# Optimization experiments

Measured on AMD Instinct MI355X. Metric: run time of the kernel, lower is better.

Reference implementation:

```python
import jax, jax.numpy as jnp
import numpy as np

N, E, D, H, L = 50000, 800000, 64, 128, 3  # nodes, edges, embed dim, mlp hidden (2*D), layers
HDIM, EDIM, G = 8, 8, 10
EPS_MSG = 1e-7
BN_EPS = 1e-5
LN_EPS = 1e-5


def setup_inputs() -> dict:
    key = jax.random.key(0)
    ks = jax.random.split(key, 12)
    s = lambda f: 1.0 / np.sqrt(f)
    return {
        "x": jax.random.normal(ks[0], (N, HDIM), jnp.float32),
        "edge_index": jax.random.randint(ks[1], (2, E), 0, N, dtype=jnp.int32),
        "edge_attr": jax.random.normal(ks[2], (E, EDIM), jnp.float32),
        "node_W": jax.random.normal(ks[3], (HDIM, D), jnp.float32) * s(HDIM),
        "node_b": jnp.zeros((D,), jnp.float32),
        "edge_W": jax.random.normal(ks[4], (EDIM, D), jnp.float32) * s(EDIM),
        "edge_b": jnp.zeros((D,), jnp.float32),
        "bn_gamma": jnp.ones((L, D), jnp.float32),
        "bn_beta": jnp.zeros((L, D), jnp.float32),
        "t": jnp.ones((L,), jnp.float32),
        "W1": jax.random.normal(ks[5], (L, D, H), jnp.float32) * s(D),
        "b1": jnp.zeros((L, H), jnp.float32),
        "ln_g": jnp.ones((L, H), jnp.float32),
        "ln_b": jnp.zeros((L, H), jnp.float32),
        "W2": jax.random.normal(ks[6], (L, H, D), jnp.float32) * s(H),
        "b2": jnp.zeros((L, D), jnp.float32),
        "num_graphs": G,
    }


def _layer(h, src, dst, e, g, b, t_i, W1i, b1i, lg, lb, W2i, b2i):
    # DeepGCNLayer 'res+': out = x + conv(relu(BN(x)))
    mu = h.mean(0)
    var = h.var(0)  # biased, as torch BN normalization
    hn = jax.nn.relu((h - mu) / jnp.sqrt(var + BN_EPS) * g + b)
    # GENConv message: relu(x_j + edge_attr) + eps
    msg = jax.nn.relu(hn[src] + e) + EPS_MSG  # [E, D]
    # softmax aggregation per destination node, per channel, with temperature t
    logits = msg * t_i
    m = jax.ops.segment_max(logits, dst, num_segments=N)
    m = jnp.where(jnp.isfinite(m), m, 0.0)
    a = jnp.exp(logits - m[dst])
    denom = jax.ops.segment_sum(a, dst, num_segments=N)
    agg = jax.ops.segment_sum(a * msg, dst, num_segments=N)
    agg = agg / jnp.maximum(denom, 1e-16)
    out = agg + hn  # GENConv root residual
    # GENConv MLP [D, 2D, D]: Linear -> LayerNorm -> ReLU -> Linear
    y = out @ W1i + b1i
    mu2 = y.mean(-1, keepdims=True)
    var2 = y.var(-1, keepdims=True)
    y = (y - mu2) / jnp.sqrt(var2 + LN_EPS) * lg + lb
    y = jax.nn.relu(y)
    y = y @ W2i + b2i
    return h + y


def reference(x, edge_index, edge_attr, node_W, node_b, edge_W, edge_b,
              bn_gamma, bn_beta, t, W1, b1, ln_g, ln_b, W2, b2, num_graphs):
    h = x @ node_W + node_b
    e = edge_attr @ edge_W + edge_b
    src, dst = edge_index[0], edge_index[1]
    for i in range(L):
        h = _layer(h, src, dst, e, bn_gamma[i], bn_beta[i], t[i],
                   W1[i], b1[i], ln_g[i], ln_b[i], W2[i], b2[i])
    return h.reshape(num_graphs, -1, D)
```

## Files before the change

### kernel.cpp

```cpp
#include <hip/hip_runtime.h>
#include <hip/hip_bf16.h>
#include <hip/hip_fp16.h>

constexpr int HDIM = 8;
constexpr int EDIM = 8;

typedef _Float16 half8 __attribute__((ext_vector_type(8)));
typedef _Float16 h2f16 __attribute__((ext_vector_type(2)));
typedef float f32x4 __attribute__((ext_vector_type(4)));
union H8U { uint4 u; half8 h; };
union H2U { unsigned u; h2f16 h; };

__device__ __forceinline__ unsigned pack2h(float a, float b) {
  __half2 h = __floats2half2_rn(a, b);
  union { __half2 h2; unsigned u; } u;
  u.h2 = h;
  return u.u;
}

__device__ __forceinline__ h2f16 u2h(unsigned v) {
  H2U u; u.u = v; return u.h;
}

__global__ __launch_bounds__(256) void init_h_stats_kernel(
    const float* __restrict__ x, const float* __restrict__ W, const float* __restrict__ b,
    unsigned short* __restrict__ h, float* __restrict__ sums, int* __restrict__ deg, int n) {
  __shared__ float reds[256], redq[256];
  int tid = threadIdx.x, lane = tid & 63;
  int gtid = blockIdx.x * 256 + tid;
  for (int i = gtid; i < n; i += 512 * 256) deg[i] = 0;
  float wc[HDIM];
#pragma unroll
  for (int k = 0; k < HDIM; ++k) wc[k] = W[k * 64 + lane];
  float bc = b[lane];
  float s = 0.f, q = 0.f;
  int total = n * 64;
  for (int gid = gtid; gid < total; gid += 512 * 256) {
    int row = gid >> 6;
    const float* xr = x + (size_t)row * HDIM;
    float acc = bc;
#pragma unroll
    for (int k = 0; k < HDIM; ++k) acc = fmaf(xr[k], wc[k], acc);
    h[gid] = __half_as_ushort(__float2half(acc));
    s += acc;
    q = fmaf(acc, acc, q);
  }
  reds[tid] = s; redq[tid] = q;
  __syncthreads();
  if (tid < 64) {
    float S = reds[tid] + reds[64 + tid] + reds[128 + tid] + reds[192 + tid];
    float Q = redq[tid] + redq[64 + tid] + redq[128 + tid] + redq[192 + tid];
    int slot = blockIdx.x & 7;
    atomicAdd(&sums[slot * 128 + tid], S);
    atomicAdd(&sums[slot * 128 + 64 + tid], Q);
  }
}

__global__ void deg_kernel(const int* __restrict__ dst, int* __restrict__ deg,
                           int* __restrict__ idxw, int E) {
  int e = blockIdx.x * 256 + threadIdx.x;
  if (e < E) idxw[e] = atomicAdd(&deg[dst[e]], 1);
}

__global__ __launch_bounds__(256) void scan_part_kernel(const int* __restrict__ deg,
                                                        int* __restrict__ partials, int n) {
  __shared__ int sh[256];
  int tid = threadIdx.x, idx = blockIdx.x * 256 + tid;
  int v = (idx < n) ? deg[idx] : 0;
  sh[tid] = v;
  __syncthreads();
  for (int o = 128; o > 0; o >>= 1) {
    if (tid < o) sh[tid] += sh[tid + o];
    __syncthreads();
  }
  if (tid == 0) partials[blockIdx.x] = sh[0];
}

__global__ __launch_bounds__(1024) void scan_top_kernel(int* __restrict__ partials, int nb) {
  __shared__ int sh[1024];
  int tid = threadIdx.x;
  int v = (tid < nb) ? partials[tid] : 0;
  sh[tid] = v;
  __syncthreads();
  for (int o = 1; o < 1024; o <<= 1) {
    int a = (tid >= o) ? sh[tid - o] : 0;
    __syncthreads();
    sh[tid] += a;
    __syncthreads();
  }
  if (tid < nb) partials[tid] = sh[tid] - v;
}

__global__ __launch_bounds__(256) void scan_fill_kernel(
    const int* __restrict__ deg, const int* __restrict__ partials,
    int* __restrict__ rowstart, int n, int total) {
  __shared__ int sh[256];
  int tid = threadIdx.x, idx = blockIdx.x * 256 + tid;
  int v = (idx < n) ? deg[idx] : 0;
  sh[tid] = v;
  __syncthreads();
  for (int o = 1; o < 256; o <<= 1) {
    int a = (tid >= o) ? sh[tid - o] : 0;
    __syncthreads();
    sh[tid] += a;
    __syncthreads();
  }
  if (idx < n) rowstart[idx] = partials[blockIdx.x] + sh[tid] - v;
  if (blockIdx.x == 0 && tid == 0) rowstart[n] = total;
}

__global__ void fill_kernel(const int* __restrict__ src, const int* __restrict__ dst,
                            const int* __restrict__ idxw, const int* __restrict__ rowstart,
                            const float* __restrict__ edge_attr, char* __restrict__ recs, int E) {
  int e = blockIdx.x * 256 + threadIdx.x;
  if (e >= E) return;
  int d = dst[e];
  int slot = rowstart[d] + idxw[e];
  const float4* ap = (const float4*)(edge_attr + (size_t)e * EDIM);
  float4 a = ap[0], c = ap[1];
  uint4 rv;
  rv.x = pack2h(a.x, a.y);
  rv.y = pack2h(a.z, a.w);
  rv.z = pack2h(c.x, c.y);
  rv.w = pack2h(c.z, c.w);
  char* rb = recs + (size_t)slot * 32;
  *(uint4*)rb = rv;
  *(int*)(rb + 16) = src[e];
}

__global__ __launch_bounds__(256) void aggregate_kernel(
    const unsigned short* __restrict__ h, const float* __restrict__ sums,
    const float* __restrict__ bn_g, const float* __restrict__ bn_b,
    const int* __restrict__ rowstart, const char* __restrict__ recs,
    const float* __restrict__ edge_W, const float* __restrict__ edge_b,
    const float* __restrict__ t, unsigned short* __restrict__ out, int n, float invN) {
  int lane = threadIdx.x & 63;
  int node = blockIdx.x * 4 + (threadIdx.x >> 6);
  if (node >= n) return;
  float ssum = 0.f, qsum = 0.f;
#pragma unroll
  for (int k = 0; k < 8; ++k) {
    ssum += sums[k * 128 + lane];
    qsum += sums[k * 128 + 64 + lane];
  }
  float mu = ssum * invN;
  float var = qsum * invN - mu * mu;
  float aa = rsqrtf(var + 1e-5f) * bn_g[lane];
  float cc = bn_b[lane] - mu * aa;
  h2f16 wc2[4];
#pragma unroll
  for (int k = 0; k < 4; ++k) {
    H2U u;
    u.u = pack2h(edge_W[(2 * k) * 64 + lane], edge_W[(2 * k + 1) * 64 + lane]);
    wc2[k] = u.h;
  }
  float eb = edge_b[lane];
  float tt2 = t[0] * 1.44269504088896f;
  int s0 = __builtin_amdgcn_readfirstlane(rowstart[node]);
  int s1 = __builtin_amdgcn_readfirstlane(rowstart[node + 1]);
  const char* hB = (const char*)h;
  const unsigned lane2 = (unsigned)lane * 2u;
  float hd;
  {
    unsigned o = (unsigned)node * 128u + lane2;
    hd = fmaxf(fmaf(__half2float(__ushort_as_half(*(const unsigned short*)(hB + o))), aa, cc), 0.f);
  }
  float den0 = 0.f, num0 = 0.f, den1 = 0.f, num1 = 0.f;
#define EDGE_STEP(HU, RV, DEN, NUM)                                            \
  {                                                                            \
    float ev = __builtin_amdgcn_fdot2(u2h(RV.x), wc2[0], eb, false);           \
    ev = __builtin_amdgcn_fdot2(u2h(RV.y), wc2[1], ev, false);                 \
    ev = __builtin_amdgcn_fdot2(u2h(RV.z), wc2[2], ev, false);                 \
    ev = __builtin_amdgcn_fdot2(u2h(RV.w), wc2[3], ev, false);                 \
    float hnv = fmaxf(fmaf(__half2float(__ushort_as_half(HU)), aa, cc), 0.f);  \
    float m = fmaxf(hnv + ev, 0.f);                                            \
    float p = exp2f(m * tt2);                                                  \
    DEN += p;                                                                  \
    NUM = fmaf(p, m, NUM);                                                     \
  }
#define GATHER(I) (*(const unsigned short*)(hB + ((unsigned)(I) * 128u + lane2)))
  int j = s0;
  for (; j + 8 <= s1; j += 8) {
    unsigned jb = (unsigned)j * 32u;
    uint4 r0 = *(const uint4*)(recs + jb);
    uint4 r1 = *(const uint4*)(recs + jb + 32);
    uint4 r2 = *(const uint4*)(recs + jb + 64);
    uint4 r3 = *(const uint4*)(recs + jb + 96);
    uint4 r4 = *(const uint4*)(recs + jb + 128);
    uint4 r5 = *(const uint4*)(recs + jb + 160);
    uint4 r6 = *(const uint4*)(recs + jb + 192);
    uint4 r7 = *(const uint4*)(recs + jb + 224);
    int i0 = *(const int*)(recs + jb + 16);
    int i1 = *(const int*)(recs + jb + 48);
    int i2 = *(const int*)(recs + jb + 80);
    int i3 = *(const int*)(recs + jb + 112);
    int i4 = *(const int*)(recs + jb + 144);
    int i5 = *(const int*)(recs + jb + 176);
    int i6 = *(const int*)(recs + jb + 208);
    int i7 = *(const int*)(recs + jb + 240);
    unsigned short u0 = GATHER(i0);
    unsigned short u1 = GATHER(i1);
    unsigned short u2 = GATHER(i2);
    unsigned short u3 = GATHER(i3);
    unsigned short u4 = GATHER(i4);
    unsigned short u5 = GATHER(i5);
    unsigned short u6 = GATHER(i6);
    unsigned short u7 = GATHER(i7);
    EDGE_STEP(u0, r0, den0, num0)
    EDGE_STEP(u1, r1, den1, num1)
    EDGE_STEP(u2, r2, den0, num0)
    EDGE_STEP(u3, r3, den1, num1)
    EDGE_STEP(u4, r4, den0, num0)
    EDGE_STEP(u5, r5, den1, num1)
    EDGE_STEP(u6, r6, den0, num0)
    EDGE_STEP(u7, r7, den1, num1)
  }
  for (; j + 4 <= s1; j += 4) {
    unsigned jb = (unsigned)j * 32u;
    uint4 r0 = *(const uint4*)(recs + jb);
    uint4 r1 = *(const uint4*)(recs + jb + 32);
    uint4 r2 = *(const uint4*)(recs + jb + 64);
    uint4 r3 = *(const uint4*)(recs + jb + 96);
    int i0 = *(const int*)(recs + jb + 16);
    int i1 = *(const int*)(recs + jb + 48);
    int i2 = *(const int*)(recs + jb + 80);
    int i3 = *(const int*)(recs + jb + 112);
    unsigned short u0 = GATHER(i0);
    unsigned short u1 = GATHER(i1);
    unsigned short u2 = GATHER(i2);
    unsigned short u3 = GATHER(i3);
    EDGE_STEP(u0, r0, den0, num0)
    EDGE_STEP(u1, r1, den1, num1)
    EDGE_STEP(u2, r2, den0, num0)
    EDGE_STEP(u3, r3, den1, num1)
  }
  for (; j < s1; ++j) {
    unsigned jb = (unsigned)j * 32u;
    uint4 r0 = *(const uint4*)(recs + jb);
    int i0 = *(const int*)(recs + jb + 16);
    unsigned short u0 = GATHER(i0);
    EDGE_STEP(u0, r0, den0, num0)
  }
#undef GATHER
#undef EDGE_STEP
  float den = den0 + den1, num = num0 + num1;
  float res = num / fmaxf(den, 1e-16f) + 1e-7f + hd;
  {
    unsigned o = (unsigned)node * 128u + lane2;
    *(unsigned short*)((char*)out + o) = __half_as_ushort(__float2half(res));
  }
}

__global__ __launch_bounds__(256) void mlp_mfma_kernel(
    const unsigned short* __restrict__ outv, const unsigned short* __restrict__ h_in,
    const float* __restrict__ W1, const float* __restrict__ b1,
    const float* __restrict__ lng, const float* __restrict__ lnb,
    const float* __restrict__ W2, const float* __restrict__ b2,
    unsigned short* __restrict__ hout16, float* __restrict__ hout32,
    float* __restrict__ nextsums, int n) {
  __shared__ uint4 lds[2560];
  const int tid = threadIdx.x;
  const int wv = tid >> 6, l = tid & 63;
  const int n0 = blockIdx.x * 64;
  uint4* XA = lds;
  uint4* WB = lds + 512;
  uint4* ZF = lds + 1536;
#pragma unroll
  for (int i = 0; i < 2; ++i) {
    int c = tid + i * 256;
    int node = c >> 3, k8 = c & 7;
    int nd = n0 + node;
    uint4 u;
    if (nd < n) {
      u = *(const uint4*)(outv + (size_t)nd * 64 + k8 * 8);
    } else {
      u = make_uint4(0, 0, 0, 0);
    }
    int mt = node >> 4, kt = k8 >> 2;
    int lanep = ((k8 & 3) << 4) | (node & 15);
    XA[(mt * 2 + kt) * 64 + lanep] = u;
  }
#pragma unroll
  for (int i = 0; i < 4; ++i) {
    int c = tid + i * 256;
    int fid = c >> 6, lp = c & 63;
    int nt = fid >> 1, kt = fid & 1;
    int ncol = (nt << 4) | (lp & 15);
    int k0 = kt * 32 + (lp >> 4) * 8;
    half8 hv;
#pragma unroll
    for (int j = 0; j < 8; ++j) hv[j] = (_Float16)W1[(size_t)(k0 + j) * 128 + ncol];
    H8U u; u.h = hv;
    WB[fid * 64 + lp] = u.u;
  }
  __syncthreads();
  f32x4 cfr[8];
#pragma unroll
  for (int nt = 0; nt < 8; ++nt) cfr[nt] = (f32x4){0.f, 0.f, 0.f, 0.f};
  {
    H8U a0, a1;
    a0.u = XA[(wv * 2 + 0) * 64 + l];
    a1.u = XA[(wv * 2 + 1) * 64 + l];
#pragma unroll
    for (int nt = 0; nt < 8; ++nt) {
      H8U b0, b1u;
      b0.u = WB[(nt * 2 + 0) * 64 + l];
      b1u.u = WB[(nt * 2 + 1) * 64 + l];
      cfr[nt] = __builtin_amdgcn_mfma_f32_16x16x32_f16(a0.h, b0.h, cfr[nt], 0, 0, 0);
      cfr[nt] = __builtin_amdgcn_mfma_f32_16x16x32_f16(a1.h, b1u.h, cfr[nt], 0, 0, 0);
    }
  }
  int col = l & 15;
  float s4[4] = {0.f, 0.f, 0.f, 0.f}, q4[4] = {0.f, 0.f, 0.f, 0.f};
#pragma unroll
  for (int nt = 0; nt < 8; ++nt) {
    float bb = b1[nt * 16 + col];
#pragma unroll
    for (int r = 0; r < 4; ++r) {
      float v = cfr[nt][r] + bb;
      cfr[nt][r] = v;
      s4[r] += v;
      q4[r] = fmaf(v, v, q4[r]);
    }
  }
#pragma unroll
  for (int off = 1; off < 16; off <<= 1) {
#pragma unroll
    for (int r = 0; r < 4; ++r) {
      s4[r] += __shfl_xor(s4[r], off, 64);
      q4[r] += __shfl_xor(q4[r], off, 64);
    }
  }
  float mu4[4], rs4[4];
#pragma unroll
  for (int r = 0; r < 4; ++r) {
    float mu = s4[r] * (1.f / 128.f);
    float var = q4[r] * (1.f / 128.f) - mu * mu;
    mu4[r] = mu;
    rs4[r] = rsqrtf(var + 1e-5f);
  }
  {
    unsigned short* ZB = (unsigned short*)ZF;
#pragma unroll
    for (int nt = 0; nt < 8; ++nt) {
      int ch = nt * 16 + col;
      int kt2 = ch >> 5, kl = ch & 31;
      float g = lng[ch], bb = lnb[ch];
#pragma unroll
      for (int r = 0; r < 4; ++r) {
        int row = (l >> 4) * 4 + r;
        float zv = fmaxf((cfr[nt][r] - mu4[r]) * rs4[r] * g + bb, 0.f);
        int lanep = ((kl >> 3) << 4) | row;
        ZB[((wv * 4 + kt2) * 64 + lanep) * 8 + (kl & 7)] = __half_as_ushort(__float2half(zv));
      }
    }
  }
  __syncthreads();
#pragma unroll
  for (int i = 0; i < 4; ++i) {
    int c = tid + i * 256;
    int fid = c >> 6, lp = c & 63;
    int nt2 = fid >> 2, kt2 = fid & 3;
    int ncol = (nt2 << 4) | (lp & 15);
    int k0 = kt2 * 32 + (lp >> 4) * 8;
    half8 hv;
#pragma unroll
    for (int j = 0; j < 8; ++j) hv[j] = (_Float16)W2[(size_t)(k0 + j) * 64 + ncol];
    H8U u; u.h = hv;
    WB[fid * 64 + lp] = u.u;
  }
  __syncthreads();
  f32x4 dfr[4];
#pragma unroll
  for (int nt2 = 0; nt2 < 4; ++nt2) dfr[nt2] = (f32x4){0.f, 0.f, 0.f, 0.f};
  {
    H8U za[4];
#pragma unroll
    for (int kt2 = 0; kt2 < 4; ++kt2) za[kt2].u = ZF[(wv * 4 + kt2) * 64 + l];
#pragma unroll
    for (int nt2 = 0; nt2 < 4; ++nt2) {
#pragma unroll
      for (int kt2 = 0; kt2 < 4; ++kt2) {
        H8U bu;
        bu.u = WB[(nt2 * 4 + kt2) * 64 + l];
        dfr[nt2] = __builtin_amdgcn_mfma_f32_16x16x32_f16(za[kt2].h, bu.h, dfr[nt2], 0, 0, 0);
      }
    }
  }
  float ssum[4] = {0.f, 0.f, 0.f, 0.f}, qsum[4] = {0.f, 0.f, 0.f, 0.f};
#pragma unroll
  for (int nt2 = 0; nt2 < 4; ++nt2) {
    int ch2 = nt2 * 16 + col;
    float bb = b2[ch2];
#pragma unroll
    for (int r = 0; r < 4; ++r) {
      int nd = n0 + wv * 16 + (l >> 4) * 4 + r;
      if (nd < n) {
        float hv = __half2float(__ushort_as_half(h_in[(size_t)nd * 64 + ch2]));
        float v = hv + dfr[nt2][r] + bb;
        if (hout32 != nullptr) {
          hout32[(size_t)nd * 64 + ch2] = v;
        } else {
          hout16[(size_t)nd * 64 + ch2] = __half_as_ushort(__float2half(v));
        }
        ssum[nt2] += v;
        qsum[nt2] = fmaf(v, v, qsum[nt2]);
      }
    }
  }
  if (nextsums != nullptr) {
#pragma unroll
    for (int nt2 = 0; nt2 < 4; ++nt2) {
      ssum[nt2] += __shfl_xor(ssum[nt2], 16, 64);
      ssum[nt2] += __shfl_xor(ssum[nt2], 32, 64);
      qsum[nt2] += __shfl_xor(qsum[nt2], 16, 64);
      qsum[nt2] += __shfl_xor(qsum[nt2], 32, 64);
    }
    float* SS = (float*)(ZF + wv * 256);
    if (l < 16) {
#pragma unroll
      for (int nt2 = 0; nt2 < 4; ++nt2) {
        SS[nt2 * 16 + l] = ssum[nt2];
        SS[64 + nt2 * 16 + l] = qsum[nt2];
      }
    }
    __syncthreads();
    if (tid < 64) {
      float S = 0.f, Q = 0.f;
#pragma unroll
      for (int w = 0; w < 4; ++w) {
        const float* P = (const float*)(ZF + w * 256);
        S += P[tid];
        Q += P[64 + tid];
      }
      int slot = blockIdx.x & 7;
      atomicAdd(&nextsums[slot * 128 + tid], S);
      atomicAdd(&nextsums[slot * 128 + 64 + tid], Q);
    }
  }
}

extern "C" void kernel_launch(void* const* d_in, const int* in_sizes, int n_in,
                              void* d_out, int out_size, void* d_ws, size_t ws_size,
                              hipStream_t stream) {
  const float* x = (const float*)d_in[0];
  const int* edge_index = (const int*)d_in[1];
  const float* edge_attr = (const float*)d_in[2];
  const float* node_W = (const float*)d_in[3];
  const float* node_b = (const float*)d_in[4];
  const float* edge_W = (const float*)d_in[5];
  const float* edge_b = (const float*)d_in[6];
  const float* bn_g = (const float*)d_in[7];
  const float* bn_b = (const float*)d_in[8];
  const float* t = (const float*)d_in[9];
  const float* W1 = (const float*)d_in[10];
  const float* b1 = (const float*)d_in[11];
  const float* ln_g = (const float*)d_in[12];
  const float* ln_b = (const float*)d_in[13];
  const float* W2 = (const float*)d_in[14];
  const float* b2 = (const float*)d_in[15];

  int N = in_sizes[0] / HDIM;
  int E = in_sizes[1] / 2;
  const int* srcp = edge_index;
  const int* dstp = edge_index + E;

  char* ws = (char*)d_ws;
  size_t off = 0;
  auto alloc = [&](size_t bytes) {
    char* p = ws + off;
    off = (off + bytes + 255) & ~(size_t)255;
    return p;
  };
  int* deg = (int*)alloc((size_t)N * 4);
  int* rowstart = (int*)alloc(((size_t)N + 1) * 4);
  int* idxw = (int*)alloc((size_t)E * 4);
  int* partials = (int*)alloc(1024 * 4);
  float* bnsums = (float*)alloc(3 * 1024 * 4);
  char* recs = (char*)alloc((size_t)E * 32);
  unsigned short* h = (unsigned short*)alloc((size_t)N * 64 * 2);
  unsigned short* outv = (unsigned short*)alloc((size_t)N * 64 * 2);
  (void)ws_size; (void)n_in; (void)out_size;

  int nb = (N + 255) / 256;
  hipMemsetAsync(bnsums, 0, 3 * 1024 * 4, stream);
  init_h_stats_kernel<<<512, 256, 0, stream>>>(x, node_W, node_b, h, bnsums, deg, N);
  deg_kernel<<<(E + 255) / 256, 256, 0, stream>>>(dstp, deg, idxw, E);
  scan_part_kernel<<<nb, 256, 0, stream>>>(deg, partials, N);
  scan_top_kernel<<<1, 1024, 0, stream>>>(partials, nb);
  scan_fill_kernel<<<nb, 256, 0, stream>>>(deg, partials, rowstart, N, E);
  fill_kernel<<<(E + 255) / 256, 256, 0, stream>>>(srcp, dstp, idxw, rowstart, edge_attr, recs, E);

  float invN = 1.0f / (float)N;
  int mlp_blocks = (N + 63) / 64;
  for (int l = 0; l < 3; ++l) {
    aggregate_kernel<<<(N + 3) / 4, 256, 0, stream>>>(
        h, bnsums + l * 1024, bn_g + l * 64, bn_b + l * 64, rowstart, recs,
        edge_W, edge_b, t + l, outv, N, invN);
    unsigned short* h16 = (l == 2) ? nullptr : h;
    float* h32 = (l == 2) ? (float*)d_out : nullptr;
    float* nxt = (l == 2) ? nullptr : (bnsums + (l + 1) * 1024);
    mlp_mfma_kernel<<<mlp_blocks, 256, 0, stream>>>(outv, h, W1 + (size_t)l * 8192, b1 + l * 128,
                                                    ln_g + l * 128, ln_b + l * 128,
                                                    W2 + (size_t)l * 8192, b2 + l * 64,
                                                    h16, h32, nxt, N);
  }
}
```

Baseline: 252.3 us.

## Fuse preprocessing kernels, use nontemporal record loads, two nodes per wave in aggregation

Degree counting moves into the init kernel and deg zeroing into the single memset, made possible by placing bnsums next to deg. The top-level scan is folded into scan_fill, with each block rescanning the partials itself. Together these remove two launches. The aggregate kernel now handles two nodes per wavefront, amortising the BN/weight setup, and loads edge records with nontemporal hints to avoid polluting cache. The risks are lower parallelism in aggregation and the scan_fill assumption that nb is at most 256, which holds for N=50000.

```diff
diff --git a/kernel.cpp b/kernel.cpp
--- a/kernel.cpp
+++ b/kernel.cpp
@@ -8,6 +8,7 @@
 typedef _Float16 half8 __attribute__((ext_vector_type(8)));
 typedef _Float16 h2f16 __attribute__((ext_vector_type(2)));
 typedef float f32x4 __attribute__((ext_vector_type(4)));
+typedef unsigned u32x4 __attribute__((ext_vector_type(4)));
 union H8U { uint4 u; half8 h; };
 union H2U { unsigned u; h2f16 h; };
 
@@ -24,11 +25,13 @@
 
 __global__ __launch_bounds__(256) void init_h_stats_kernel(
     const float* __restrict__ x, const float* __restrict__ W, const float* __restrict__ b,
-    unsigned short* __restrict__ h, float* __restrict__ sums, int* __restrict__ deg, int n) {
+    unsigned short* __restrict__ h, float* __restrict__ sums,
+    const int* __restrict__ dst, int* __restrict__ idxw, int* __restrict__ deg,
+    int n, int E) {
   __shared__ float reds[256], redq[256];
   int tid = threadIdx.x, lane = tid & 63;
   int gtid = blockIdx.x * 256 + tid;
-  for (int i = gtid; i < n; i += 512 * 256) deg[i] = 0;
+  for (int e = gtid; e < E; e += 512 * 256) idxw[e] = atomicAdd(&deg[dst[e]], 1);
   float wc[HDIM];
 #pragma unroll
   for (int k = 0; k < HDIM; ++k) wc[k] = W[k * 64 + lane];
@@ -54,12 +57,6 @@
     atomicAdd(&sums[slot * 128 + tid], S);
     atomicAdd(&sums[slot * 128 + 64 + tid], Q);
   }
-}
-
-__global__ void deg_kernel(const int* __restrict__ dst, int* __restrict__ deg,
-                           int* __restrict__ idxw, int E) {
-  int e = blockIdx.x * 256 + threadIdx.x;
-  if (e < E) idxw[e] = atomicAdd(&deg[dst[e]], 1);
 }
 
 __global__ __launch_bounds__(256) void scan_part_kernel(const int* __restrict__ deg,
@@ -76,36 +73,27 @@
   if (tid == 0) partials[blockIdx.x] = sh[0];
 }
 
-__global__ __launch_bounds__(1024) void scan_top_kernel(int* __restrict__ partials, int nb) {
-  __shared__ int sh[1024];
-  int tid = threadIdx.x;
-  int v = (tid < nb) ? partials[tid] : 0;
-  sh[tid] = v;
-  __syncthreads();
-  for (int o = 1; o < 1024; o <<= 1) {
-    int a = (tid >= o) ? sh[tid - o] : 0;
-    __syncthreads();
-    sh[tid] += a;
-    __syncthreads();
-  }
-  if (tid < nb) partials[tid] = sh[tid] - v;
-}
-
 __global__ __launch_bounds__(256) void scan_fill_kernel(
     const int* __restrict__ deg, const int* __restrict__ partials,
-    int* __restrict__ rowstart, int n, int total) {
+    int* __restrict__ rowstart, int n, int total, int nb) {
+  __shared__ int tp[256];
   __shared__ int sh[256];
   int tid = threadIdx.x, idx = blockIdx.x * 256 + tid;
+  int pv = (tid < nb) ? partials[tid] : 0;
+  tp[tid] = pv;
   int v = (idx < n) ? deg[idx] : 0;
   sh[tid] = v;
   __syncthreads();
   for (int o = 1; o < 256; o <<= 1) {
-    int a = (tid >= o) ? sh[tid - o] : 0;
+    int a1 = (tid >= o) ? tp[tid - o] : 0;
+    int a2 = (tid >= o) ? sh[tid - o] : 0;
     __syncthreads();
-    sh[tid] += a;
+    tp[tid] += a1;
+    sh[tid] += a2;
     __syncthreads();
   }
-  if (idx < n) rowstart[idx] = partials[blockIdx.x] + sh[tid] - v;
+  int base = (blockIdx.x == 0) ? 0 : tp[blockIdx.x - 1];
+  if (idx < n) rowstart[idx] = base + sh[tid] - v;
   if (blockIdx.x == 0 && tid == 0) rowstart[n] = total;
 }
 
@@ -128,38 +116,12 @@
   *(int*)(rb + 16) = src[e];
 }
 
-__global__ __launch_bounds__(256) void aggregate_kernel(
-    const unsigned short* __restrict__ h, const float* __restrict__ sums,
-    const float* __restrict__ bn_g, const float* __restrict__ bn_b,
+__device__ __forceinline__ float agg_one(
+    int node, unsigned lane2, const char* __restrict__ hB,
     const int* __restrict__ rowstart, const char* __restrict__ recs,
-    const float* __restrict__ edge_W, const float* __restrict__ edge_b,
-    const float* __restrict__ t, unsigned short* __restrict__ out, int n, float invN) {
-  int lane = threadIdx.x & 63;
-  int node = blockIdx.x * 4 + (threadIdx.x >> 6);
-  if (node >= n) return;
-  float ssum = 0.f, qsum = 0.f;
-#pragma unroll
-  for (int k = 0; k < 8; ++k) {
-    ssum += sums[k * 128 + lane];
-    qsum += sums[k * 128 + 64 + lane];
-  }
-  float mu = ssum * invN;
-  float var = qsum * invN - mu * mu;
-  float aa = rsqrtf(var + 1e-5f) * bn_g[lane];
-  float cc = bn_b[lane] - mu * aa;
-  h2f16 wc2[4];
-#pragma unroll
-  for (int k = 0; k < 4; ++k) {
-    H2U u;
-    u.u = pack2h(edge_W[(2 * k) * 64 + lane], edge_W[(2 * k + 1) * 64 + lane]);
-    wc2[k] = u.h;
-  }
-  float eb = edge_b[lane];
-  float tt2 = t[0] * 1.44269504088896f;
+    const h2f16* wc2, float eb, float tt2, float aa, float cc) {
   int s0 = __builtin_amdgcn_readfirstlane(rowstart[node]);
   int s1 = __builtin_amdgcn_readfirstlane(rowstart[node + 1]);
-  const char* hB = (const char*)h;
-  const unsigned lane2 = (unsigned)lane * 2u;
   float hd;
   {
     unsigned o = (unsigned)node * 128u + lane2;
@@ -179,25 +141,27 @@
     NUM = fmaf(p, m, NUM);                                                     \
   }
 #define GATHER(I) (*(const unsigned short*)(hB + ((unsigned)(I) * 128u + lane2)))
+#define NT4(OFF) __builtin_nontemporal_load((const u32x4*)(recs + jb + (OFF)))
+#define NTI(OFF) __builtin_nontemporal_load((const int*)(recs + jb + (OFF)))
   int j = s0;
   for (; j + 8 <= s1; j += 8) {
     unsigned jb = (unsigned)j * 32u;
-    uint4 r0 = *(const uint4*)(recs + jb);
-    uint4 r1 = *(const uint4*)(recs + jb + 32);
-    uint4 r2 = *(const uint4*)(recs + jb + 64);
-    uint4 r3 = *(const uint4*)(recs + jb + 96);
-    uint4 r4 = *(const uint4*)(recs + jb + 128);
-    uint4 r5 = *(const uint4*)(recs + jb + 160);
-    uint4 r6 = *(const uint4*)(recs + jb + 192);
-    uint4 r7 = *(const uint4*)(recs + jb + 224);
-    int i0 = *(const int*)(recs + jb + 16);
-    int i1 = *(const int*)(recs + jb + 48);
-    int i2 = *(const int*)(recs + jb + 80);
-    int i3 = *(const int*)(recs + jb + 112);
-    int i4 = *(const int*)(recs + jb + 144);
-    int i5 = *(const int*)(recs + jb + 176);
-    int i6 = *(const int*)(recs + jb + 208);
-    int i7 = *(const int*)(recs + jb + 240);
+    u32x4 r0 = NT4(0);
+    u32x4 r1 = NT4(32);
+    u32x4 r2 = NT4(64);
+    u32x4 r3 = NT4(96);
+    u32x4 r4 = NT4(128);
+    u32x4 r5 = NT4(160);
+    u32x4 r6 = NT4(192);
+    u32x4 r7 = NT4(224);
+    int i0 = NTI(16);
+    int i1 = NTI(48);
+    int i2 = NTI(80);
+    int i3 = NTI(112);
+    int i4 = NTI(144);
+    int i5 = NTI(176);
+    int i6 = NTI(208);
+    int i7 = NTI(240);
     unsigned short u0 = GATHER(i0);
     unsigned short u1 = GATHER(i1);
     unsigned short u2 = GATHER(i2);
@@ -217,14 +181,14 @@
   }
   for (; j + 4 <= s1; j += 4) {
     unsigned jb = (unsigned)j * 32u;
-    uint4 r0 = *(const uint4*)(recs + jb);
-    uint4 r1 = *(const uint4*)(recs + jb + 32);
-    uint4 r2 = *(const uint4*)(recs + jb + 64);
-    uint4 r3 = *(const uint4*)(recs + jb + 96);
-    int i0 = *(const int*)(recs + jb + 16);
-    int i1 = *(const int*)(recs + jb + 48);
-    int i2 = *(const int*)(recs + jb + 80);
-    int i3 = *(const int*)(recs + jb + 112);
+    u32x4 r0 = NT4(0);
+    u32x4 r1 = NT4(32);
+    u32x4 r2 = NT4(64);
+    u32x4 r3 = NT4(96);
+    int i0 = NTI(16);
+    int i1 = NTI(48);
+    int i2 = NTI(80);
+    int i3 = NTI(112);
     unsigned short u0 = GATHER(i0);
     unsigned short u1 = GATHER(i1);
     unsigned short u2 = GATHER(i2);
@@ -236,18 +200,57 @@
   }
   for (; j < s1; ++j) {
     unsigned jb = (unsigned)j * 32u;
-    uint4 r0 = *(const uint4*)(recs + jb);
-    int i0 = *(const int*)(recs + jb + 16);
+    u32x4 r0 = NT4(0);
+    int i0 = NTI(16);
     unsigned short u0 = GATHER(i0);
     EDGE_STEP(u0, r0, den0, num0)
   }
+#undef NT4
+#undef NTI
 #undef GATHER
 #undef EDGE_STEP
   float den = den0 + den1, num = num0 + num1;
-  float res = num / fmaxf(den, 1e-16f) + 1e-7f + hd;
-  {
-    unsigned o = (unsigned)node * 128u + lane2;
-    *(unsigned short*)((char*)out + o) = __half_as_ushort(__float2half(res));
+  return num / fmaxf(den, 1e-16f) + 1e-7f + hd;
+}
+
+__global__ __launch_bounds__(256) void aggregate_kernel(
+    const unsigned short* __restrict__ h, const float* __restrict__ sums,
+    const float* __restrict__ bn_g, const float* __restrict__ bn_b,
+    const int* __restrict__ rowstart, const char* __restrict__ recs,
+    const float* __restrict__ edge_W, const float* __restrict__ edge_b,
+    const float* __restrict__ t, unsigned short* __restrict__ out, int n, float invN) {
+  int lane = threadIdx.x & 63;
+  int nodeA = (blockIdx.x * 4 + (threadIdx.x >> 6)) * 2;
+  if (nodeA >= n) return;
+  int nodeB = nodeA + 1;
+  float ssum = 0.f, qsum = 0.f;
+#pragma unroll
+  for (int k = 0; k < 8; ++k) {
+    ssum += sums[k * 128 + lane];
+    qsum += sums[k * 128 + 64 + lane];
+  }
+  float mu = ssum * invN;
+  float var = qsum * invN - mu * mu;
+  float aa = rsqrtf(var + 1e-5f) * bn_g[lane];
+  float cc = bn_b[lane] - mu * aa;
+  h2f16 wc2[4];
+#pragma unroll
+  for (int k = 0; k < 4; ++k) {
+    H2U u;
+    u.u = pack2h(edge_W[(2 * k) * 64 + lane], edge_W[(2 * k + 1) * 64 + lane]);
+    wc2[k] = u.h;
+  }
+  float eb = edge_b[lane];
+  float tt2 = t[0] * 1.44269504088896f;
+  const char* hB = (const char*)h;
+  const unsigned lane2 = (unsigned)lane * 2u;
+  float resA = agg_one(nodeA, lane2, hB, rowstart, recs, wc2, eb, tt2, aa, cc);
+  *(unsigned short*)((char*)out + ((unsigned)nodeA * 128u + lane2)) =
+      __half_as_ushort(__float2half(resA));
+  if (nodeB < n) {
+    float resB = agg_one(nodeB, lane2, hB, rowstart, recs, wc2, eb, tt2, aa, cc);
+    *(unsigned short*)((char*)out + ((unsigned)nodeB * 128u + lane2)) =
+        __half_as_ushort(__float2half(resB));
   }
 }
 
@@ -472,29 +475,29 @@
     off = (off + bytes + 255) & ~(size_t)255;
     return p;
   };
+  float* bnsums = (float*)alloc(3 * 1024 * 4);
   int* deg = (int*)alloc((size_t)N * 4);
   int* rowstart = (int*)alloc(((size_t)N + 1) * 4);
   int* idxw = (int*)alloc((size_t)E * 4);
   int* partials = (int*)alloc(1024 * 4);
-  float* bnsums = (float*)alloc(3 * 1024 * 4);
   char* recs = (char*)alloc((size_t)E * 32);
   unsigned short* h = (unsigned short*)alloc((size_t)N * 64 * 2);
   unsigned short* outv = (unsigned short*)alloc((size_t)N * 64 * 2);
   (void)ws_size; (void)n_in; (void)out_size;
 
   int nb = (N + 255) / 256;
-  hipMemsetAsync(bnsums, 0, 3 * 1024 * 4, stream);
-  init_h_stats_kernel<<<512, 256, 0, stream>>>(x, node_W, node_b, h, bnsums, deg, N);
-  deg_kernel<<<(E + 255) / 256, 256, 0, stream>>>(dstp, deg, idxw, E);
+  hipMemsetAsync(bnsums, 0, 3 * 1024 * 4 + (size_t)N * 4, stream);
+  init_h_stats_kernel<<<512, 256, 0, stream>>>(x, node_W, node_b, h, bnsums,
+                                               dstp, idxw, deg, N, E);
   scan_part_kernel<<<nb, 256, 0, stream>>>(deg, partials, N);
-  scan_top_kernel<<<1, 1024, 0, stream>>>(partials, nb);
-  scan_fill_kernel<<<nb, 256, 0, stream>>>(deg, partials, rowstart, N, E);
+  scan_fill_kernel<<<nb, 256, 0, stream>>>(deg, partials, rowstart, N, E, nb);
   fill_kernel<<<(E + 255) / 256, 256, 0, stream>>>(srcp, dstp, idxw, rowstart, edge_attr, recs, E);
 
   float invN = 1.0f / (float)N;
   int mlp_blocks = (N + 63) / 64;
+  int agg_blocks = (N + 7) / 8;
   for (int l = 0; l < 3; ++l) {
-    aggregate_kernel<<<(N + 3) / 4, 256, 0, stream>>>(
+    aggregate_kernel<<<agg_blocks, 256, 0, stream>>>(
         h, bnsums + l * 1024, bn_g + l * 64, bn_b + l * 64, rowstart, recs,
         edge_W, edge_b, t + l, outv, N, invN);
     unsigned short* h16 = (l == 2) ? nullptr : h;
```

New measurement: 243.9 us. -3.3%, faster.
